# Optimization experiments

Measured on AMD Instinct MI355X. Metric: run time of the kernel, lower is better.

The kernel has to match this reference:

```python
import jax, jax.numpy as jnp
import numpy as np

N, F, C1, H, C2, E = 50000, 256, 32, 8, 16, 800000
NEG_SLOPE = 0.2


def gat_layer(x, src, dst, W, a_src, a_dst, b, heads, out_c, concat):
    n = x.shape[0]
    h = (x @ W).reshape(n, heads, out_c)               # [N,H,C]
    al_src = jnp.sum(h * a_src, axis=-1)               # [N,H]
    al_dst = jnp.sum(h * a_dst, axis=-1)               # [N,H]
    e = jax.nn.leaky_relu(al_src[src] + al_dst[dst], NEG_SLOPE)  # [E,H]
    # segment softmax over incoming edges of each dst node
    m = jax.ops.segment_max(e, dst, num_segments=n)
    e = jnp.exp(e - m[dst])
    denom = jax.ops.segment_sum(e, dst, num_segments=n)
    alpha = e / (denom[dst] + 1e-16)                   # [E,H]
    msg = h[src] * alpha[..., None]                    # [E,H,C]
    out = jax.ops.segment_sum(msg, dst, num_segments=n)
    out = out.reshape(n, heads * out_c) if concat else out.mean(axis=1)
    return out + b


def conv1d(x, w, b):
    # x: [1,C,N], w: [O,I,K], 'same' padding (K=5 -> pad 2)
    pad = (w.shape[-1] - 1) // 2
    y = jax.lax.conv_general_dilated(x, w, (1,), [(pad, pad)],
                                     dimension_numbers=('NCH', 'OIH', 'NCH'))
    return y + b[None, :, None]


def setup_inputs() -> dict:
    key = jax.random.key(0)
    ks = jax.random.split(key, 20)
    s = lambda k, shp, sc: jax.random.normal(k, shp, jnp.float32) * sc
    inp = {
        'x': jax.random.normal(ks[0], (N, F), jnp.float32),
        'edge_index': jax.random.randint(ks[1], (2, E), 0, N, jnp.int32),
        'W1': s(ks[2], (F, H * C1), 0.06),
        'a_src1': s(ks[3], (H, C1), 0.1), 'a_dst1': s(ks[4], (H, C1), 0.1),
        'b1': jnp.zeros((H * C1,), jnp.float32),
        'W2': s(ks[5], (H * C1, C2), 0.06),
        'a_src2': s(ks[6], (1, C2), 0.1), 'a_dst2': s(ks[7], (1, C2), 0.1),
        'b2': jnp.zeros((C2,), jnp.float32),
        'proj_w': s(ks[8], (C2, 1), 0.2), 'proj_b': jnp.zeros((1,), jnp.float32),
        'c1_w': s(ks[9], (C2, C2, 5), 0.1), 'c1_b': jnp.zeros((C2,), jnp.float32),
        'c2_w': s(ks[10], (C2, C2, 5), 0.1), 'c2_b': jnp.zeros((C2,), jnp.float32),
        'lin_w': s(ks[11], (2 * C2, C2), 0.15), 'lin_b': jnp.zeros((C2,), jnp.float32),
    }
    return inp


def reference(x, edge_index, W1, a_src1, a_dst1, b1, W2, a_src2, a_dst2, b2,
              proj_w, proj_b, c1_w, c1_b, c2_w, c2_b, lin_w, lin_b):
    n = x.shape[0]
    loops = jnp.arange(n, dtype=edge_index.dtype)
    src = jnp.concatenate([edge_index[0], loops])  # PyG GATConv adds self-loops
    dst = jnp.concatenate([edge_index[1], loops])

    h = jax.nn.relu(gat_layer(x, src, dst, W1, a_src1, a_dst1, b1, H, C1, True))
    x1 = gat_layer(h, src, dst, W2, a_src2, a_dst2, b2, 1, C2, False)  # [N,C2]

    g = (x1 @ proj_w + proj_b)[:, 0]                  # [N]
    sort_idx = jnp.argsort(g)
    inverse_idx = jnp.argsort(sort_idx)
    sorted_x = g[sort_idx][:, None] * x1[sort_idx]    # [N,C2]
    sx = sorted_x.T[None]                             # [1,C2,N]
    sx = jax.nn.relu(conv1d(sx, c1_w, c1_b))
    sx = conv1d(sx, c2_w, c2_b)
    x2 = sx[0].T[inverse_idx]                         # [N,C2]

    out = jnp.concatenate([x1, x2], axis=1) @ lin_w + lin_b
    return jax.nn.log_softmax(out, axis=1)
```

## Files before the change

kernel.cpp:

```cpp
#include <hip/hip_runtime.h>
#include <math.h>

#define NBUCKET 65536

__device__ __forceinline__ float leakyrelu02(float v) { return v > 0.f ? v : 0.2f * v; }

__global__ __launch_bounds__(256) void k_gemm1(const float* __restrict__ A,
                                               const float* __restrict__ B,
                                               float* __restrict__ C, int M) {
  __shared__ float As[16][132];
  __shared__ float Bs[16][132];
  const int m0 = blockIdx.x * 128;
  const int n0 = blockIdx.y * 128;
  const int tid = threadIdx.x;
  const int tm = tid & 15;
  const int tn = tid >> 4;
  float acc[8][8];
#pragma unroll
  for (int i = 0; i < 8; ++i)
#pragma unroll
    for (int j = 0; j < 8; ++j) acc[i][j] = 0.f;

  const int ar = tid & 127, aseg = (tid >> 7) * 8;
  const int br = tid >> 4, bc = (tid & 15) * 8;

  for (int k0 = 0; k0 < 256; k0 += 16) {
    float4 a0 = make_float4(0.f, 0.f, 0.f, 0.f);
    float4 a1 = make_float4(0.f, 0.f, 0.f, 0.f);
    if (m0 + ar < M) {
      const float* ap = A + (size_t)(m0 + ar) * 256 + k0 + aseg;
      a0 = *(const float4*)(ap);
      a1 = *(const float4*)(ap + 4);
    }
    As[aseg + 0][ar] = a0.x;
    As[aseg + 1][ar] = a0.y;
    As[aseg + 2][ar] = a0.z;
    As[aseg + 3][ar] = a0.w;
    As[aseg + 4][ar] = a1.x;
    As[aseg + 5][ar] = a1.y;
    As[aseg + 6][ar] = a1.z;
    As[aseg + 7][ar] = a1.w;
    const float* bp = B + (size_t)(k0 + br) * 256 + n0 + bc;
    *(float4*)&Bs[br][bc] = *(const float4*)(bp);
    *(float4*)&Bs[br][bc + 4] = *(const float4*)(bp + 4);
    __syncthreads();
#pragma unroll
    for (int kk = 0; kk < 16; ++kk) {
      float a[8], b[8];
      *(float4*)&a[0] = *(const float4*)&As[kk][tm * 4];
      *(float4*)&a[4] = *(const float4*)&As[kk][64 + tm * 4];
      *(float4*)&b[0] = *(const float4*)&Bs[kk][tn * 4];
      *(float4*)&b[4] = *(const float4*)&Bs[kk][64 + tn * 4];
#pragma unroll
      for (int i = 0; i < 8; ++i)
#pragma unroll
        for (int j = 0; j < 8; ++j) acc[i][j] += a[i] * b[j];
    }
    __syncthreads();
  }
#pragma unroll
  for (int i = 0; i < 8; ++i) {
    int m = m0 + ((i < 4) ? (tm * 4 + i) : (64 + tm * 4 + i - 4));
    if (m < M) {
      float4 o0 = make_float4(acc[i][0], acc[i][1], acc[i][2], acc[i][3]);
      float4 o1 = make_float4(acc[i][4], acc[i][5], acc[i][6], acc[i][7]);
      *(float4*)(C + (size_t)m * 256 + n0 + tn * 4) = o0;
      *(float4*)(C + (size_t)m * 256 + n0 + 64 + tn * 4) = o1;
    }
  }
}

__global__ __launch_bounds__(256) void k_al1(const float* __restrict__ h_lin,
                                             const float* __restrict__ a_src,
                                             const float* __restrict__ a_dst,
                                             float* __restrict__ als,
                                             float* __restrict__ ald, int N) {
  int gid = blockIdx.x * 256 + threadIdx.x;
  int n = gid >> 6;
  int l = threadIdx.x & 63;
  if (n >= N) return;
  float4 h4 = *(const float4*)(h_lin + (size_t)n * 256 + l * 4);
  float4 vs = *(const float4*)(a_src + l * 4);
  float4 vd = *(const float4*)(a_dst + l * 4);
  float ps = h4.x * vs.x + h4.y * vs.y + h4.z * vs.z + h4.w * vs.w;
  float pd = h4.x * vd.x + h4.y * vd.y + h4.z * vd.z + h4.w * vd.w;
  ps += __shfl_xor(ps, 1); pd += __shfl_xor(pd, 1);
  ps += __shfl_xor(ps, 2); pd += __shfl_xor(pd, 2);
  ps += __shfl_xor(ps, 4); pd += __shfl_xor(pd, 4);
  if ((l & 7) == 0) {
    als[(size_t)n * 8 + (l >> 3)] = ps;
    ald[(size_t)n * 8 + (l >> 3)] = pd;
  }
}

__global__ __launch_bounds__(256) void k_hist(const int* __restrict__ ei,
                                              int* __restrict__ counts, int E, int N) {
  int e = blockIdx.x * 256 + threadIdx.x;
  if (e >= E + N) return;
  int d = (e < E) ? ei[E + e] : (e - E);
  atomicAdd(&counts[d], 1);
}

__global__ __launch_bounds__(1024) void k_scan(const int* __restrict__ counts,
                                               int* __restrict__ offsets,
                                               int* __restrict__ cursor, int chunk) {
  __shared__ int part[1024];
  const int t = threadIdx.x;
  const int base = t * chunk;
  int ssum = 0;
  for (int i = 0; i < chunk; i += 4) {
    int4 v = *(const int4*)(counts + base + i);
    ssum += v.x + v.y + v.z + v.w;
  }
  part[t] = ssum;
  __syncthreads();
  for (int d = 1; d < 1024; d <<= 1) {
    int v = (t >= d) ? part[t - d] : 0;
    __syncthreads();
    part[t] += v;
    __syncthreads();
  }
  int run = (t == 0) ? 0 : part[t - 1];
  for (int i = 0; i < chunk; i += 4) {
    int4 v = *(const int4*)(counts + base + i);
    int4 o;
    o.x = run; run += v.x;
    o.y = run; run += v.y;
    o.z = run; run += v.z;
    o.w = run; run += v.w;
    *(int4*)(offsets + base + i) = o;
    if (cursor) *(int4*)(cursor + base + i) = o;
  }
  if (t == 1023) offsets[1024 * chunk] = run;
}

__global__ __launch_bounds__(256) void k_scatter_ew(
    const int* __restrict__ ei, const float* __restrict__ als1,
    const float* __restrict__ ald1, int* __restrict__ cursor,
    int* __restrict__ csr_src, int* __restrict__ csr_dst,
    float* __restrict__ ew, int E, int N) {
  int e = blockIdx.x * 256 + threadIdx.x;
  if (e >= E + N) return;
  int d, s;
  if (e < E) { d = ei[E + e]; s = ei[e]; }
  else { d = e - E; s = d; }
  int pos = atomicAdd(&cursor[d], 1);
  csr_src[pos] = s;
  csr_dst[pos] = d;
  float4 as0 = *(const float4*)(als1 + (size_t)s * 8);
  float4 as1 = *(const float4*)(als1 + (size_t)s * 8 + 4);
  float4 ad0 = *(const float4*)(ald1 + (size_t)d * 8);
  float4 ad1 = *(const float4*)(ald1 + (size_t)d * 8 + 4);
  float4 w0, w1;
  w0.x = expf(leakyrelu02(as0.x + ad0.x));
  w0.y = expf(leakyrelu02(as0.y + ad0.y));
  w0.z = expf(leakyrelu02(as0.z + ad0.z));
  w0.w = expf(leakyrelu02(as0.w + ad0.w));
  w1.x = expf(leakyrelu02(as1.x + ad1.x));
  w1.y = expf(leakyrelu02(as1.y + ad1.y));
  w1.z = expf(leakyrelu02(as1.z + ad1.z));
  w1.w = expf(leakyrelu02(as1.w + ad1.w));
  *(float4*)(ew + (size_t)pos * 8) = w0;
  *(float4*)(ew + (size_t)pos * 8 + 4) = w1;
}

__global__ __launch_bounds__(256) void k_ew2(const int* __restrict__ csr_src,
                                             const int* __restrict__ csr_dst,
                                             const float* __restrict__ als2,
                                             const float* __restrict__ ald2,
                                             float* __restrict__ ew2, int Etot) {
  int t = blockIdx.x * 256 + threadIdx.x;
  if (t >= Etot) return;
  ew2[t] = expf(leakyrelu02(als2[csr_src[t]] + ald2[csr_dst[t]]));
}

#define RB(i) ((i) + ((i) >> 3))

__global__ __launch_bounds__(256) void k_gat1(
    const float* __restrict__ h_lin, const float* __restrict__ ew,
    const float* __restrict__ b1, const int* __restrict__ offsets,
    const int* __restrict__ csr_src, const float* __restrict__ W2,
    const float* __restrict__ a_src2, const float* __restrict__ a_dst2,
    float* __restrict__ h2, float* __restrict__ als2, float* __restrict__ ald2, int N) {
  __shared__ float rowbuf[4][292];

  const int w = threadIdx.x >> 6;
  const int l = threadIdx.x & 63;
  const int half = l >> 5;
  const int li = l & 31;
  const int h3 = li >> 2;
  const int n = blockIdx.x * 4 + w;
  if (n >= N) return;

  const int off = offsets[n];
  const int deg = offsets[n + 1] - off;
  const float* hb = h_lin + li * 8;

  float c0 = 0.f, c1 = 0.f, c2 = 0.f, c3 = 0.f, c4 = 0.f, c5 = 0.f, c6 = 0.f, c7 = 0.f;
  float sw = 0.f;
  int e = 0;
  for (; e + 8 <= deg; e += 8) {
    const int p0 = off + e + half;
    int s0 = csr_src[p0];
    int s1 = csr_src[p0 + 2];
    int s2 = csr_src[p0 + 4];
    int s3 = csr_src[p0 + 6];
    float w0 = ew[(size_t)p0 * 8 + h3];
    float w1 = ew[(size_t)(p0 + 2) * 8 + h3];
    float w2v = ew[(size_t)(p0 + 4) * 8 + h3];
    float w3 = ew[(size_t)(p0 + 6) * 8 + h3];
    const float* r0p = hb + (size_t)s0 * 256;
    const float* r1p = hb + (size_t)s1 * 256;
    const float* r2p = hb + (size_t)s2 * 256;
    const float* r3p = hb + (size_t)s3 * 256;
    float4 r0a = *(const float4*)(r0p), r0b = *(const float4*)(r0p + 4);
    float4 r1a = *(const float4*)(r1p), r1b = *(const float4*)(r1p + 4);
    float4 r2a = *(const float4*)(r2p), r2b = *(const float4*)(r2p + 4);
    float4 r3a = *(const float4*)(r3p), r3b = *(const float4*)(r3p + 4);
    sw += (w0 + w1) + (w2v + w3);
    c0 += w0 * r0a.x + w1 * r1a.x + w2v * r2a.x + w3 * r3a.x;
    c1 += w0 * r0a.y + w1 * r1a.y + w2v * r2a.y + w3 * r3a.y;
    c2 += w0 * r0a.z + w1 * r1a.z + w2v * r2a.z + w3 * r3a.z;
    c3 += w0 * r0a.w + w1 * r1a.w + w2v * r2a.w + w3 * r3a.w;
    c4 += w0 * r0b.x + w1 * r1b.x + w2v * r2b.x + w3 * r3b.x;
    c5 += w0 * r0b.y + w1 * r1b.y + w2v * r2b.y + w3 * r3b.y;
    c6 += w0 * r0b.z + w1 * r1b.z + w2v * r2b.z + w3 * r3b.z;
    c7 += w0 * r0b.w + w1 * r1b.w + w2v * r2b.w + w3 * r3b.w;
  }
  for (; e < deg; e += 2) {
    int ee = e + half;
    if (ee < deg) {
      int p = off + ee;
      int s = csr_src[p];
      float ww = ew[(size_t)p * 8 + h3];
      const float* rp = hb + (size_t)s * 256;
      float4 ra = *(const float4*)(rp), rb = *(const float4*)(rp + 4);
      sw += ww;
      c0 += ww * ra.x; c1 += ww * ra.y; c2 += ww * ra.z; c3 += ww * ra.w;
      c4 += ww * rb.x; c5 += ww * rb.y; c6 += ww * rb.z; c7 += ww * rb.w;
    }
  }
  c0 += __shfl_xor(c0, 32); c1 += __shfl_xor(c1, 32);
  c2 += __shfl_xor(c2, 32); c3 += __shfl_xor(c3, 32);
  c4 += __shfl_xor(c4, 32); c5 += __shfl_xor(c5, 32);
  c6 += __shfl_xor(c6, 32); c7 += __shfl_xor(c7, 32);
  sw += __shfl_xor(sw, 32);
  const float inv = 1.f / (sw + 1e-16f);

  if (half == 0) {
    float4 ba = *(const float4*)(b1 + li * 8);
    float4 bbv = *(const float4*)(b1 + li * 8 + 4);
    rowbuf[w][RB(li * 8 + 0)] = fmaxf(c0 * inv + ba.x, 0.f);
    rowbuf[w][RB(li * 8 + 1)] = fmaxf(c1 * inv + ba.y, 0.f);
    rowbuf[w][RB(li * 8 + 2)] = fmaxf(c2 * inv + ba.z, 0.f);
    rowbuf[w][RB(li * 8 + 3)] = fmaxf(c3 * inv + ba.w, 0.f);
    rowbuf[w][RB(li * 8 + 4)] = fmaxf(c4 * inv + bbv.x, 0.f);
    rowbuf[w][RB(li * 8 + 5)] = fmaxf(c5 * inv + bbv.y, 0.f);
    rowbuf[w][RB(li * 8 + 6)] = fmaxf(c6 * inv + bbv.z, 0.f);
    rowbuf[w][RB(li * 8 + 7)] = fmaxf(c7 * inv + bbv.w, 0.f);
  }
  asm volatile("s_waitcnt lgkmcnt(0)" ::: "memory");

  const int o = l & 15;
  const int grp = l >> 4;
  float a2 = 0.f;
#pragma unroll 8
  for (int t = 0; t < 64; ++t) {
    int cc = grp * 64 + ((t + grp * 8) & 63);
    a2 += rowbuf[w][RB(cc)] * W2[cc * 16 + o];
  }
  a2 += __shfl_xor(a2, 16);
  a2 += __shfl_xor(a2, 32);

  if (l < 16) {
    h2[(size_t)n * 16 + l] = a2;
    float ps = a2 * a_src2[l];
    float pd = a2 * a_dst2[l];
    ps += __shfl_xor(ps, 1); pd += __shfl_xor(pd, 1);
    ps += __shfl_xor(ps, 2); pd += __shfl_xor(pd, 2);
    ps += __shfl_xor(ps, 4); pd += __shfl_xor(pd, 4);
    ps += __shfl_xor(ps, 8); pd += __shfl_xor(pd, 8);
    if (l == 0) { als2[n] = ps; ald2[n] = pd; }
  }
}

__global__ __launch_bounds__(256) void k_gat2(
    const float* __restrict__ h2, const float* __restrict__ ew2,
    const float* __restrict__ b2, const float* __restrict__ proj_w,
    const float* __restrict__ proj_b, const int* __restrict__ offsets,
    const int* __restrict__ csr_src, float* __restrict__ x1,
    float* __restrict__ g, unsigned long long* __restrict__ keys,
    int* __restrict__ bhist, int N) {
  const int w = threadIdx.x >> 6;
  const int l = threadIdx.x & 63;
  const int n = blockIdx.x * 4 + w;
  if (n >= N) return;
  const int off = offsets[n];
  const int deg = offsets[n + 1] - off;
  const int slot = l >> 4;
  const int c = l & 15;

  float acc = 0.f, sw = 0.f;
  int e0 = 0;
  for (; e0 + 8 <= deg; e0 += 8) {
    int pA = off + e0 + slot;
    int pB = off + e0 + 4 + slot;
    int sA = csr_src[pA];
    int sB = csr_src[pB];
    float wA = ew2[pA];
    float wB = ew2[pB];
    float hA = h2[(size_t)sA * 16 + c];
    float hB = h2[(size_t)sB * 16 + c];
    sw += wA + wB;
    acc += wA * hA + wB * hB;
  }
  for (; e0 < deg; e0 += 4) {
    int e = e0 + slot;
    if (e < deg) {
      int p = off + e;
      int s = csr_src[p];
      float v = ew2[p];
      sw += v;
      acc += v * h2[(size_t)s * 16 + c];
    }
  }
  acc += __shfl_xor(acc, 16); sw += __shfl_xor(sw, 16);
  acc += __shfl_xor(acc, 32); sw += __shfl_xor(sw, 32);
  float x1v = acc / (sw + 1e-16f) + b2[c];

  float pg = x1v * proj_w[c];
  pg += __shfl_xor(pg, 1);
  pg += __shfl_xor(pg, 2);
  pg += __shfl_xor(pg, 4);
  pg += __shfl_xor(pg, 8);
  if (l < 16) x1[(size_t)n * 16 + l] = x1v;
  if (l == 0) {
    float gv = pg + proj_b[0];
    g[n] = gv;
    unsigned u = __float_as_uint(gv);
    u = (u & 0x80000000u) ? ~u : (u | 0x80000000u);
    keys[n] = (((unsigned long long)u) << 32) | (unsigned)n;
    atomicAdd(&bhist[u >> 16], 1);
  }
}

__global__ __launch_bounds__(256) void k_bscatter(const unsigned long long* __restrict__ keys,
                                                  int* __restrict__ cursor,
                                                  unsigned long long* __restrict__ bkeys, int N) {
  int n = blockIdx.x * 256 + threadIdx.x;
  if (n >= N) return;
  unsigned long long k = keys[n];
  int b = (int)(k >> 48);
  int pos = atomicAdd(&cursor[b], 1);
  bkeys[pos] = k;
}

__global__ __launch_bounds__(256) void k_brank(const unsigned long long* __restrict__ bkeys,
                                               const int* __restrict__ boffs,
                                               const float* __restrict__ g,
                                               const float* __restrict__ x1,
                                               int* __restrict__ rank,
                                               float* __restrict__ sortedv, int N) {
  int pos = blockIdx.x * 256 + threadIdx.x;
  if (pos >= N) return;
  unsigned long long k = bkeys[pos];
  int b = (int)(k >> 48);
  int lo = boffs[b], hi = boffs[b + 1];
  int r = lo;
  for (int j = lo; j < hi; ++j) r += (bkeys[j] < k) ? 1 : 0;
  int idx = (int)(unsigned)(k & 0xffffffffull);
  rank[idx] = r;
  float gv = g[idx];
#pragma unroll
  for (int c = 0; c < 16; c += 4) {
    float4 v = *(const float4*)(x1 + (size_t)idx * 16 + c);
    float4 o = make_float4(gv * v.x, gv * v.y, gv * v.z, gv * v.w);
    *(float4*)(sortedv + (size_t)r * 16 + c) = o;
  }
}

__global__ __launch_bounds__(256) void k_conv(const float* __restrict__ in,
                                              const float* __restrict__ wgt,
                                              const float* __restrict__ bias,
                                              float* __restrict__ out, int N, int relu) {
  __shared__ float s[260][17];
  __shared__ float ws[1280];
  __shared__ float bs[16];
  const int p0 = blockIdx.x * 256;
  for (int i = threadIdx.x; i < 1280; i += 256) ws[i] = wgt[i];
  if (threadIdx.x < 16) bs[threadIdx.x] = bias[threadIdx.x];
  for (int idx = threadIdx.x; idx < 260 * 16; idx += 256) {
    int lp = idx >> 4, c = idx & 15;
    int gp = p0 - 2 + lp;
    s[lp][c] = (gp >= 0 && gp < N) ? in[(size_t)gp * 16 + c] : 0.f;
  }
  __syncthreads();
  const int p = p0 + threadIdx.x;
  if (p >= N) return;
  float acc[16];
#pragma unroll
  for (int o = 0; o < 16; ++o) acc[o] = bs[o];
  for (int k = 0; k < 5; ++k) {
    for (int c = 0; c < 16; ++c) {
      float xv = s[threadIdx.x + k][c];
#pragma unroll
      for (int o = 0; o < 16; ++o) acc[o] += ws[(o * 16 + c) * 5 + k] * xv;
    }
  }
#pragma unroll
  for (int o = 0; o < 16; ++o) {
    float v = acc[o];
    if (relu) v = fmaxf(v, 0.f);
    out[(size_t)p * 16 + o] = v;
  }
}

__global__ __launch_bounds__(256) void k_final(
    const float* __restrict__ x1, const float* __restrict__ c2out,
    const int* __restrict__ rank, const float* __restrict__ lin_w,
    const float* __restrict__ lin_b, float* __restrict__ out, int N) {
  __shared__ float lw[512];
  __shared__ float lb[16];
  for (int i = threadIdx.x; i < 512; i += 256) lw[i] = lin_w[i];
  if (threadIdx.x < 16) lb[threadIdx.x] = lin_b[threadIdx.x];
  __syncthreads();
  const int n = blockIdx.x * 256 + threadIdx.x;
  if (n >= N) return;
  float xa[16], xb[16];
  const int r = rank[n];
#pragma unroll
  for (int c = 0; c < 16; c += 4) {
    float4 va = *(const float4*)(x1 + (size_t)n * 16 + c);
    float4 vb = *(const float4*)(c2out + (size_t)r * 16 + c);
    xa[c] = va.x; xa[c + 1] = va.y; xa[c + 2] = va.z; xa[c + 3] = va.w;
    xb[c] = vb.x; xb[c + 1] = vb.y; xb[c + 2] = vb.z; xb[c + 3] = vb.w;
  }
  float z[16];
#pragma unroll
  for (int o = 0; o < 16; ++o) z[o] = lb[o];
#pragma unroll
  for (int c = 0; c < 16; ++c) {
    float va = xa[c], vb = xb[c];
#pragma unroll
    for (int o = 0; o < 16; ++o) z[o] += va * lw[c * 16 + o] + vb * lw[(16 + c) * 16 + o];
  }
  float m = z[0];
#pragma unroll
  for (int o = 1; o < 16; ++o) m = fmaxf(m, z[o]);
  float ssum = 0.f;
#pragma unroll
  for (int o = 0; o < 16; ++o) ssum += expf(z[o] - m);
  float lse = m + logf(ssum);
#pragma unroll
  for (int o = 0; o < 16; ++o) out[(size_t)n * 16 + o] = z[o] - lse;
}

extern "C" void kernel_launch(void* const* d_in, const int* in_sizes, int n_in,
                              void* d_out, int out_size, void* d_ws, size_t ws_size,
                              hipStream_t stream) {
  const float* x = (const float*)d_in[0];
  const int* ei = (const int*)d_in[1];
  const float* W1 = (const float*)d_in[2];
  const float* a_src1 = (const float*)d_in[3];
  const float* a_dst1 = (const float*)d_in[4];
  const float* b1 = (const float*)d_in[5];
  const float* W2 = (const float*)d_in[6];
  const float* a_src2 = (const float*)d_in[7];
  const float* a_dst2 = (const float*)d_in[8];
  const float* b2 = (const float*)d_in[9];
  const float* proj_w = (const float*)d_in[10];
  const float* proj_b = (const float*)d_in[11];
  const float* c1_w = (const float*)d_in[12];
  const float* c1_b = (const float*)d_in[13];
  const float* c2_w = (const float*)d_in[14];
  const float* c2_b = (const float*)d_in[15];
  const float* lin_w = (const float*)d_in[16];
  const float* lin_b = (const float*)d_in[17];
  float* out = (float*)d_out;

  const int N = in_sizes[0] / 256;
  const int E = in_sizes[1] / 2;
  const int Etot = E + N;

  int chunk = (N + 1023) / 1024;
  chunk = (chunk + 3) & ~3;
  const int Npad = 1024 * chunk;

  char* ws = (char*)d_ws;
  size_t off = 0;
  auto alloc = [&](size_t bytes) -> void* {
    void* p = ws + off;
    off = (off + bytes + 255) & ~(size_t)255;
    return p;
  };
  float* h_lin = (float*)alloc((size_t)N * 256 * 4);
  float* als1 = (float*)alloc((size_t)N * 8 * 4);
  float* ald1 = (float*)alloc((size_t)N * 8 * 4);
  int* counts = (int*)alloc((size_t)Npad * 4);
  int* offsets = (int*)alloc((size_t)(Npad + 1) * 4);
  int* cursor = (int*)alloc((size_t)Npad * 4);
  int* csr_src = (int*)alloc((size_t)Etot * 4);
  int* csr_dst = (int*)alloc((size_t)Etot * 4);
  float* ew = (float*)alloc((size_t)Etot * 8 * 4);
  float* ew2 = (float*)alloc((size_t)Etot * 4);
  float* h2 = (float*)alloc((size_t)N * 16 * 4);
  float* als2 = (float*)alloc((size_t)N * 4);
  float* ald2 = (float*)alloc((size_t)N * 4);
  float* x1 = (float*)alloc((size_t)N * 16 * 4);
  float* gbuf = (float*)alloc((size_t)N * 4);
  unsigned long long* keys = (unsigned long long*)alloc((size_t)N * 8);
  int* bhist = (int*)alloc((size_t)NBUCKET * 4);
  int* boffs = (int*)alloc((size_t)(NBUCKET + 1) * 4);
  int* bcursor = (int*)alloc((size_t)NBUCKET * 4);
  unsigned long long* bkeys = (unsigned long long*)alloc((size_t)N * 8);
  int* rank = (int*)alloc((size_t)N * 4);
  float* sortedv = (float*)alloc((size_t)N * 16 * 4);
  float* c1out = (float*)alloc((size_t)N * 16 * 4);
  float* c2out = (float*)alloc((size_t)N * 16 * 4);
  if (off > ws_size) return;

  hipMemsetAsync(counts, 0, (size_t)Npad * 4, stream);
  hipMemsetAsync(bhist, 0, (size_t)NBUCKET * 4, stream);

  dim3 gg((N + 127) / 128, 2);
  k_gemm1<<<gg, 256, 0, stream>>>(x, W1, h_lin, N);
  k_al1<<<(N + 3) / 4, 256, 0, stream>>>(h_lin, a_src1, a_dst1, als1, ald1, N);
  k_hist<<<(Etot + 255) / 256, 256, 0, stream>>>(ei, counts, E, N);
  k_scan<<<1, 1024, 0, stream>>>(counts, offsets, cursor, chunk);
  k_scatter_ew<<<(Etot + 255) / 256, 256, 0, stream>>>(ei, als1, ald1, cursor,
                                                       csr_src, csr_dst, ew, E, N);
  k_gat1<<<(N + 3) / 4, 256, 0, stream>>>(h_lin, ew, b1, offsets, csr_src,
                                          W2, a_src2, a_dst2, h2, als2, ald2, N);
  k_ew2<<<(Etot + 255) / 256, 256, 0, stream>>>(csr_src, csr_dst, als2, ald2, ew2, Etot);
  k_gat2<<<(N + 3) / 4, 256, 0, stream>>>(h2, ew2, b2, proj_w, proj_b,
                                          offsets, csr_src, x1, gbuf, keys, bhist, N);
  k_scan<<<1, 1024, 0, stream>>>(bhist, boffs, bcursor, NBUCKET / 1024);
  k_bscatter<<<(N + 255) / 256, 256, 0, stream>>>(keys, bcursor, bkeys, N);
  k_brank<<<(N + 255) / 256, 256, 0, stream>>>(bkeys, boffs, gbuf, x1, rank, sortedv, N);
  k_conv<<<(N + 255) / 256, 256, 0, stream>>>(sortedv, c1_w, c1_b, c1out, N, 1);
  k_conv<<<(N + 255) / 256, 256, 0, stream>>>(c1out, c2_w, c2_b, c2out, N, 0);
  k_final<<<(N + 255) / 256, 256, 0, stream>>>(x1, c2out, rank, lin_w, lin_b, out, N);
}
```

Before: 597.5 us.

## Restructure first GEMM to 64x64 tiles with wave-uniform B loads from global

```diff
diff --git a/kernel.cpp b/kernel.cpp
--- a/kernel.cpp
+++ b/kernel.cpp
@@ -8,65 +8,50 @@
 __global__ __launch_bounds__(256) void k_gemm1(const float* __restrict__ A,
                                                const float* __restrict__ B,
                                                float* __restrict__ C, int M) {
-  __shared__ float As[16][132];
-  __shared__ float Bs[16][132];
-  const int m0 = blockIdx.x * 128;
-  const int n0 = blockIdx.y * 128;
+  __shared__ float As[16][68];
+  const int m0 = blockIdx.x * 64;
+  const int n0 = blockIdx.y * 64;
   const int tid = threadIdx.x;
-  const int tm = tid & 15;
-  const int tn = tid >> 4;
-  float acc[8][8];
-#pragma unroll
-  for (int i = 0; i < 8; ++i)
-#pragma unroll
-    for (int j = 0; j < 8; ++j) acc[i][j] = 0.f;
-
-  const int ar = tid & 127, aseg = (tid >> 7) * 8;
-  const int br = tid >> 4, bc = (tid & 15) * 8;
+  const int l = tid & 63;
+  const int wu = __builtin_amdgcn_readfirstlane(tid >> 6);
+  const float* __restrict__ Bw = B + n0 + wu * 16;
+
+  float acc[16];
+#pragma unroll
+  for (int j = 0; j < 16; ++j) acc[j] = 0.f;
+
+  const int arow = tid & 63, akk = (tid >> 6) * 4;
 
   for (int k0 = 0; k0 < 256; k0 += 16) {
-    float4 a0 = make_float4(0.f, 0.f, 0.f, 0.f);
-    float4 a1 = make_float4(0.f, 0.f, 0.f, 0.f);
-    if (m0 + ar < M) {
-      const float* ap = A + (size_t)(m0 + ar) * 256 + k0 + aseg;
-      a0 = *(const float4*)(ap);
-      a1 = *(const float4*)(ap + 4);
-    }
-    As[aseg + 0][ar] = a0.x;
-    As[aseg + 1][ar] = a0.y;
-    As[aseg + 2][ar] = a0.z;
-    As[aseg + 3][ar] = a0.w;
-    As[aseg + 4][ar] = a1.x;
-    As[aseg + 5][ar] = a1.y;
-    As[aseg + 6][ar] = a1.z;
-    As[aseg + 7][ar] = a1.w;
-    const float* bp = B + (size_t)(k0 + br) * 256 + n0 + bc;
-    *(float4*)&Bs[br][bc] = *(const float4*)(bp);
-    *(float4*)&Bs[br][bc + 4] = *(const float4*)(bp + 4);
+    float4 av = make_float4(0.f, 0.f, 0.f, 0.f);
+    if (m0 + arow < M) av = *(const float4*)(A + (size_t)(m0 + arow) * 256 + k0 + akk);
+    As[akk + 0][arow] = av.x;
+    As[akk + 1][arow] = av.y;
+    As[akk + 2][arow] = av.z;
+    As[akk + 3][arow] = av.w;
     __syncthreads();
 #pragma unroll
     for (int kk = 0; kk < 16; ++kk) {
-      float a[8], b[8];
-      *(float4*)&a[0] = *(const float4*)&As[kk][tm * 4];
-      *(float4*)&a[4] = *(const float4*)&As[kk][64 + tm * 4];
-      *(float4*)&b[0] = *(const float4*)&Bs[kk][tn * 4];
-      *(float4*)&b[4] = *(const float4*)&Bs[kk][64 + tn * 4];
-#pragma unroll
-      for (int i = 0; i < 8; ++i)
-#pragma unroll
-        for (int j = 0; j < 8; ++j) acc[i][j] += a[i] * b[j];
+      const float* bp = Bw + (size_t)(k0 + kk) * 256;
+      float4 b0 = *(const float4*)(bp);
+      float4 b1 = *(const float4*)(bp + 4);
+      float4 b2 = *(const float4*)(bp + 8);
+      float4 b3 = *(const float4*)(bp + 12);
+      float a = As[kk][l];
+      acc[0] += a * b0.x;  acc[1] += a * b0.y;  acc[2] += a * b0.z;  acc[3] += a * b0.w;
+      acc[4] += a * b1.x;  acc[5] += a * b1.y;  acc[6] += a * b1.z;  acc[7] += a * b1.w;
+      acc[8] += a * b2.x;  acc[9] += a * b2.y;  acc[10] += a * b2.z; acc[11] += a * b2.w;
+      acc[12] += a * b3.x; acc[13] += a * b3.y; acc[14] += a * b3.z; acc[15] += a * b3.w;
     }
     __syncthreads();
   }
-#pragma unroll
-  for (int i = 0; i < 8; ++i) {
-    int m = m0 + ((i < 4) ? (tm * 4 + i) : (64 + tm * 4 + i - 4));
-    if (m < M) {
-      float4 o0 = make_float4(acc[i][0], acc[i][1], acc[i][2], acc[i][3]);
-      float4 o1 = make_float4(acc[i][4], acc[i][5], acc[i][6], acc[i][7]);
-      *(float4*)(C + (size_t)m * 256 + n0 + tn * 4) = o0;
-      *(float4*)(C + (size_t)m * 256 + n0 + 64 + tn * 4) = o1;
-    }
+  const int m = m0 + l;
+  if (m < M) {
+    float* cp = C + (size_t)m * 256 + n0 + wu * 16;
+    *(float4*)(cp + 0) = make_float4(acc[0], acc[1], acc[2], acc[3]);
+    *(float4*)(cp + 4) = make_float4(acc[4], acc[5], acc[6], acc[7]);
+    *(float4*)(cp + 8) = make_float4(acc[8], acc[9], acc[10], acc[11]);
+    *(float4*)(cp + 12) = make_float4(acc[12], acc[13], acc[14], acc[15]);
   }
 }
 
@@ -522,7 +507,7 @@
   hipMemsetAsync(counts, 0, (size_t)Npad * 4, stream);
   hipMemsetAsync(bhist, 0, (size_t)NBUCKET * 4, stream);
 
-  dim3 gg((N + 127) / 128, 2);
+  dim3 gg((N + 63) / 64, 4);
   k_gemm1<<<gg, 256, 0, stream>>>(x, W1, h_lin, N);
   k_al1<<<(N + 3) / 4, 256, 0, stream>>>(h_lin, a_src1, a_dst1, als1, ald1, N);
   k_hist<<<(Etot + 255) / 256, 256, 0, stream>>>(ei, counts, E, N);
```

After: 539.4 us. 1.11x faster.
